# Kernel optimization log

Measured on AMD Instinct MI355X. Metric: run time of the kernel, lower is better.

Reference implementation:

```python
import jax, jax.numpy as jnp
import numpy as np

N_UNITS, IN, HID, BATCH = 512, 64, 64, 512
STD = float(np.sqrt(1.0 / HID))


def setup_inputs() -> dict:
    key = jax.random.key(0)
    ks = jax.random.split(key, 16)
    d = {
        "x": jax.random.normal(ks[0], (BATCH, N_UNITS, IN), jnp.float32),
        "h": jax.random.normal(ks[1], (BATCH, N_UNITS, HID), jnp.float32),
    }
    names = ["ir", "hr", "iz", "hz", "in", "hn"]
    for i, nm in enumerate(names):
        din = IN if nm.startswith("i") else HID
        d[f"W_{nm}"] = jax.random.normal(ks[2 + 2 * i], (N_UNITS, din, HID), jnp.float32) * STD
        d[f"b_{nm}"] = jax.random.normal(ks[3 + 2 * i], (N_UNITS, HID), jnp.float32) * STD
    return d


def _uwl(x, W, b):
    # per-unit linear: (B,U,din) @ (U,din,dout) + (U,dout) -> (B,U,dout)
    return jnp.einsum("bui,uio->buo", x, W) + b


def reference(x, h, W_ir, b_ir, W_hr, b_hr, W_iz, b_iz, W_hz, b_hz, W_in, b_in, W_hn, b_hn):
    r = jax.nn.sigmoid(_uwl(x, W_ir, b_ir) + _uwl(h, W_hr, b_hr))
    z = jax.nn.sigmoid(_uwl(x, W_iz, b_iz) + _uwl(h, W_hz, b_hz))
    n = jnp.tanh(_uwl(x, W_in, b_in) + r * _uwl(h, W_hn, b_hn))
    return (1.0 - z) * n + z * h
```

## Files before the change

### kernel.cpp

```cpp
#include <hip/hip_runtime.h>
#include <cstddef>

#define BATCH 512
#define UNITS 512
#define HID   64

typedef __bf16 bf16x8 __attribute__((ext_vector_type(8)));
typedef float  f32x4  __attribute__((ext_vector_type(4)));

__device__ __forceinline__ float fast_sigmoid(float v) {
    return __builtin_amdgcn_rcpf(1.0f + __expf(-v));
}
__device__ __forceinline__ float fast_tanh(float v) {
    return 2.0f * __builtin_amdgcn_rcpf(1.0f + __expf(-2.0f * v)) - 1.0f;
}

__global__ __launch_bounds__(512, 2)
void gru_kernel(const float* __restrict__ x,    const float* __restrict__ h,
                const float* __restrict__ W_ir, const float* __restrict__ b_ir,
                const float* __restrict__ W_hr, const float* __restrict__ b_hr,
                const float* __restrict__ W_iz, const float* __restrict__ b_iz,
                const float* __restrict__ W_hz, const float* __restrict__ b_hz,
                const float* __restrict__ W_in, const float* __restrict__ b_in,
                const float* __restrict__ W_hn, const float* __restrict__ b_hn,
                float* __restrict__ out)
{
    __shared__ __align__(16) unsigned char wlds[6 * 512 * 16];
    __shared__ float blds[4][64];

    const int u    = (blockIdx.x & 7) * 64 + (blockIdx.x >> 3);
    const int tid  = threadIdx.x;
    const int lane = tid & 63;
    const int w    = tid >> 6;
    const int lr   = lane & 15;
    const int lg   = lane >> 4;

    const float* pxB = x + ((size_t)(w * 16 + lr) * UNITS + u) * HID;
    const float* phB = h + ((size_t)(w * 16 + lr) * UNITS + u) * HID;
    const size_t istep = (size_t)128 * UNITS * HID;
    const int k0 = lg * 8;
    const int k1 = 32 + lg * 8;

    f32x4 rx0, rx1, rx2, rx3, rh0, rh1, rh2, rh3;
    rx0 = *(const f32x4*)(pxB + k0);
    rx1 = *(const f32x4*)(pxB + k0 + 4);
    rx2 = *(const f32x4*)(pxB + k1);
    rx3 = *(const f32x4*)(pxB + k1 + 4);
    rh0 = *(const f32x4*)(phB + k0);
    rh1 = *(const f32x4*)(phB + k0 + 4);
    rh2 = *(const f32x4*)(phB + k1);
    rh3 = *(const f32x4*)(phB + k1 + 4);

    const float* Wg[6] = {
        W_ir + (size_t)u * 64 * 64, W_hr + (size_t)u * 64 * 64,
        W_iz + (size_t)u * 64 * 64, W_hz + (size_t)u * 64 * 64,
        W_in + (size_t)u * 64 * 64, W_hn + (size_t)u * 64 * 64 };

    {
      const int ks_s = tid >> 8;
      const int n_s  = (tid >> 6) & 3;
      const int lg_s = (tid >> 4) & 3;
      const int lr_s = tid & 15;
      const int i0   = ks_s * 32 + lg_s * 8;
      const int o_s  = n_s * 16 + lr_s;
      #pragma unroll
      for (int g = 0; g < 6; ++g) {
        const float* q = Wg[g] + (size_t)i0 * 64 + o_s;
        bf16x8 f;
        #pragma unroll
        for (int e = 0; e < 8; ++e) f[e] = (__bf16)q[(size_t)e * 64];
        *(bf16x8*)(wlds + (size_t)(g * 512 + tid) * 16) = f;
      }
    }

    if (tid < 256) {
      const int o_l = tid & 63;
      const int which = tid >> 6;
      const int o = u * 64 + o_l;
      float v;
      if      (which == 0) v = b_ir[o] + b_hr[o];
      else if (which == 1) v = b_iz[o] + b_hz[o];
      else if (which == 2) v = b_in[o];
      else                 v = b_hn[o];
      blds[which][o_l] = v;
    }

    __syncthreads();

    const f32x4 zero4 = { 0.0f, 0.0f, 0.0f, 0.0f };
    const int loff = lane * 16;

    #pragma unroll 1
    for (int it = 0; it < 4; ++it) {
      const int brow0 = it * 128 + w * 16;

      bf16x8 ax[2], ah[2];
      {
        bf16x8 f;
        #pragma unroll
        for (int e = 0; e < 4; ++e) { f[e] = (__bf16)rx0[e]; f[4+e] = (__bf16)rx1[e]; }
        ax[0] = f;
        #pragma unroll
        for (int e = 0; e < 4; ++e) { f[e] = (__bf16)rx2[e]; f[4+e] = (__bf16)rx3[e]; }
        ax[1] = f;
        #pragma unroll
        for (int e = 0; e < 4; ++e) { f[e] = (__bf16)rh0[e]; f[4+e] = (__bf16)rh1[e]; }
        ah[0] = f;
        #pragma unroll
        for (int e = 0; e < 4; ++e) { f[e] = (__bf16)rh2[e]; f[4+e] = (__bf16)rh3[e]; }
        ah[1] = f;
      }

      if (it < 3) {
        const float* px = pxB + (size_t)(it + 1) * istep;
        const float* ph = phB + (size_t)(it + 1) * istep;
        rx0 = *(const f32x4*)(px + k0);
        rx1 = *(const f32x4*)(px + k0 + 4);
        rx2 = *(const f32x4*)(px + k1);
        rx3 = *(const f32x4*)(px + k1 + 4);
        rh0 = *(const f32x4*)(ph + k0);
        rh1 = *(const f32x4*)(ph + k0 + 4);
        rh2 = *(const f32x4*)(ph + k1);
        rh3 = *(const f32x4*)(ph + k1 + 4);
      }

      #pragma unroll 1
      for (int n = 0; n < 4; ++n) {
        const int o = n * 16 + lr;

        float hv[4];
        #pragma unroll
        for (int j = 0; j < 4; ++j) {
          const int row = brow0 + lg * 4 + j;
          hv[j] = h[((size_t)row * UNITS + u) * HID + o];
        }
        const float br = blds[0][o];
        const float bz = blds[1][o];
        const float bi = blds[2][o];
        const float bh = blds[3][o];

        f32x4 accr = zero4, accz = zero4, acca = zero4, accb = zero4;
        #pragma unroll
        for (int ks = 0; ks < 2; ++ks) {
          const unsigned char* bp = wlds + ks * 4096 + n * 1024 + loff;
          bf16x8 b0 = *(const bf16x8*)(bp + 0 * 8192);
          bf16x8 b1 = *(const bf16x8*)(bp + 1 * 8192);
          bf16x8 b2 = *(const bf16x8*)(bp + 2 * 8192);
          bf16x8 b3 = *(const bf16x8*)(bp + 3 * 8192);
          bf16x8 b4 = *(const bf16x8*)(bp + 4 * 8192);
          bf16x8 b5 = *(const bf16x8*)(bp + 5 * 8192);
          accr = __builtin_amdgcn_mfma_f32_16x16x32_bf16(ax[ks], b0, accr, 0, 0, 0);
          accr = __builtin_amdgcn_mfma_f32_16x16x32_bf16(ah[ks], b1, accr, 0, 0, 0);
          accz = __builtin_amdgcn_mfma_f32_16x16x32_bf16(ax[ks], b2, accz, 0, 0, 0);
          accz = __builtin_amdgcn_mfma_f32_16x16x32_bf16(ah[ks], b3, accz, 0, 0, 0);
          acca = __builtin_amdgcn_mfma_f32_16x16x32_bf16(ax[ks], b4, acca, 0, 0, 0);
          accb = __builtin_amdgcn_mfma_f32_16x16x32_bf16(ah[ks], b5, accb, 0, 0, 0);
        }

        #pragma unroll
        for (int j = 0; j < 4; ++j) {
          const int row = brow0 + lg * 4 + j;
          const size_t idx = ((size_t)row * UNITS + u) * HID + o;
          const float rv = fast_sigmoid(accr[j] + br);
          const float zv = fast_sigmoid(accz[j] + bz);
          const float nv = fast_tanh(acca[j] + bi + rv * (accb[j] + bh));
          out[idx] = (1.0f - zv) * nv + zv * hv[j];
        }
      }
    }
}

extern "C" void kernel_launch(void* const* d_in, const int* in_sizes, int n_in,
                              void* d_out, int out_size, void* d_ws, size_t ws_size,
                              hipStream_t stream) {
    const float* x    = (const float*)d_in[0];
    const float* h    = (const float*)d_in[1];
    const float* W_ir = (const float*)d_in[2];
    const float* b_ir = (const float*)d_in[3];
    const float* W_hr = (const float*)d_in[4];
    const float* b_hr = (const float*)d_in[5];
    const float* W_iz = (const float*)d_in[6];
    const float* b_iz = (const float*)d_in[7];
    const float* W_hz = (const float*)d_in[8];
    const float* b_hz = (const float*)d_in[9];
    const float* W_in = (const float*)d_in[10];
    const float* b_in = (const float*)d_in[11];
    const float* W_hn = (const float*)d_in[12];
    const float* b_hn = (const float*)d_in[13];
    float* out = (float*)d_out;

    gru_kernel<<<dim3(UNITS), dim3(512), 0, stream>>>(
        x, h, W_ir, b_ir, W_hr, b_hr, W_iz, b_iz, W_hz, b_hz,
        W_in, b_in, W_hn, b_hn, out);
}
```

Before: 55.71 us.

## Transpose MFMA output for vector stores and reuse staged h from LDS

Swaps the MFMA A/B operands so each lane's accumulator holds four consecutive output columns of one batch row. This allows one 16-byte store per lane instead of four scalar stores. The gating residual now takes h from a bf16 copy staged in LDS instead of re-reading fp32 h from global memory, and biases are loaded as vectors. The aim is fewer memory instructions and less redundant global traffic. The cost is extra LDS use and a bf16-rounded h in the final blend, which lowers accuracy.

```diff
diff --git a/kernel.cpp b/kernel.cpp
--- a/kernel.cpp
+++ b/kernel.cpp
@@ -6,6 +6,7 @@
 #define HID   64
 
 typedef __bf16 bf16x8 __attribute__((ext_vector_type(8)));
+typedef __bf16 bf16x4 __attribute__((ext_vector_type(4)));
 typedef float  f32x4  __attribute__((ext_vector_type(4)));
 
 __device__ __forceinline__ float fast_sigmoid(float v) {
@@ -27,6 +28,7 @@
 {
     __shared__ __align__(16) unsigned char wlds[6 * 512 * 16];
     __shared__ float blds[4][64];
+    __shared__ __align__(16) __bf16 hlds[8][16][72];
 
     const int u    = (blockIdx.x & 7) * 64 + (blockIdx.x >> 3);
     const int tid  = threadIdx.x;
@@ -124,20 +126,18 @@
         rh3 = *(const f32x4*)(ph + k1 + 4);
       }
 
+      *(bf16x8*)(&hlds[w][lr][lg * 8])      = ah[0];
+      *(bf16x8*)(&hlds[w][lr][32 + lg * 8]) = ah[1];
+
+      __builtin_amdgcn_sched_barrier(0);
+
       #pragma unroll 1
       for (int n = 0; n < 4; ++n) {
-        const int o = n * 16 + lr;
-
-        float hv[4];
-        #pragma unroll
-        for (int j = 0; j < 4; ++j) {
-          const int row = brow0 + lg * 4 + j;
-          hv[j] = h[((size_t)row * UNITS + u) * HID + o];
-        }
-        const float br = blds[0][o];
-        const float bz = blds[1][o];
-        const float bi = blds[2][o];
-        const float bh = blds[3][o];
+        const f32x4 brv = *(const f32x4*)(&blds[0][n * 16 + lg * 4]);
+        const f32x4 bzv = *(const f32x4*)(&blds[1][n * 16 + lg * 4]);
+        const f32x4 biv = *(const f32x4*)(&blds[2][n * 16 + lg * 4]);
+        const f32x4 bhv = *(const f32x4*)(&blds[3][n * 16 + lg * 4]);
+        const bf16x4 hq = *(const bf16x4*)(&hlds[w][lr][n * 16 + lg * 4]);
 
         f32x4 accr = zero4, accz = zero4, acca = zero4, accb = zero4;
         #pragma unroll
@@ -149,23 +149,24 @@
           bf16x8 b3 = *(const bf16x8*)(bp + 3 * 8192);
           bf16x8 b4 = *(const bf16x8*)(bp + 4 * 8192);
           bf16x8 b5 = *(const bf16x8*)(bp + 5 * 8192);
-          accr = __builtin_amdgcn_mfma_f32_16x16x32_bf16(ax[ks], b0, accr, 0, 0, 0);
-          accr = __builtin_amdgcn_mfma_f32_16x16x32_bf16(ah[ks], b1, accr, 0, 0, 0);
-          accz = __builtin_amdgcn_mfma_f32_16x16x32_bf16(ax[ks], b2, accz, 0, 0, 0);
-          accz = __builtin_amdgcn_mfma_f32_16x16x32_bf16(ah[ks], b3, accz, 0, 0, 0);
-          acca = __builtin_amdgcn_mfma_f32_16x16x32_bf16(ax[ks], b4, acca, 0, 0, 0);
-          accb = __builtin_amdgcn_mfma_f32_16x16x32_bf16(ah[ks], b5, accb, 0, 0, 0);
+          accr = __builtin_amdgcn_mfma_f32_16x16x32_bf16(b0, ax[ks], accr, 0, 0, 0);
+          accr = __builtin_amdgcn_mfma_f32_16x16x32_bf16(b1, ah[ks], accr, 0, 0, 0);
+          accz = __builtin_amdgcn_mfma_f32_16x16x32_bf16(b2, ax[ks], accz, 0, 0, 0);
+          accz = __builtin_amdgcn_mfma_f32_16x16x32_bf16(b3, ah[ks], accz, 0, 0, 0);
+          acca = __builtin_amdgcn_mfma_f32_16x16x32_bf16(b4, ax[ks], acca, 0, 0, 0);
+          accb = __builtin_amdgcn_mfma_f32_16x16x32_bf16(b5, ah[ks], accb, 0, 0, 0);
         }
 
+        f32x4 ov;
         #pragma unroll
         for (int j = 0; j < 4; ++j) {
-          const int row = brow0 + lg * 4 + j;
-          const size_t idx = ((size_t)row * UNITS + u) * HID + o;
-          const float rv = fast_sigmoid(accr[j] + br);
-          const float zv = fast_sigmoid(accz[j] + bz);
-          const float nv = fast_tanh(acca[j] + bi + rv * (accb[j] + bh));
-          out[idx] = (1.0f - zv) * nv + zv * hv[j];
+          const float rv = fast_sigmoid(accr[j] + brv[j]);
+          const float zv = fast_sigmoid(accz[j] + bzv[j]);
+          const float nv = fast_tanh(acca[j] + biv[j] + rv * (accb[j] + bhv[j]));
+          ov[j] = (1.0f - zv) * nv + zv * (float)hq[j];
         }
+        float* po = out + ((size_t)(brow0 + lr) * UNITS + u) * HID + n * 16 + lg * 4;
+        *(f32x4*)po = ov;
       }
     }
 }
```

Result: faster. 47.56 us (median of 2 runs) (-14.6%).
